# Performance work log

Hardware: AMD Instinct MI355X
Metric: run time of the kernel (lower is better)

Reference implementation:

```python
import jax, jax.numpy as jnp
import numpy as np

IN_DIMS = 32
HID = 64
N_HIDDEN = 5  # tcnn n_hidden_layers = hidden_layers + 1 = 5
OUT_DIMS = 3
BATCH = 2097152


def setup_inputs() -> dict:
    key = jax.random.key(0)
    ks = jax.random.split(key, N_HIDDEN + 2)
    x = jax.random.normal(ks[0], (BATCH, IN_DIMS), dtype=jnp.float32)
    # tcnn FullyFusedMLP has no biases; Kaiming-ish init scale
    W0 = jax.random.normal(ks[1], (IN_DIMS, HID), dtype=jnp.float32) * (1.0 / np.sqrt(IN_DIMS))
    Wh = jax.random.normal(ks[2], (N_HIDDEN - 1, HID, HID), dtype=jnp.float32) * (1.0 / np.sqrt(HID))
    Wo = jax.random.normal(ks[3], (HID, OUT_DIMS), dtype=jnp.float32) * (1.0 / np.sqrt(HID))
    return {"x": x, "W0": W0, "Wh": Wh, "Wo": Wo}


def reference(x, W0, Wh, Wo):
    # input layer -> ReLU
    h = jax.nn.relu(x @ W0)  # [B, 64]
    # 4 more hidden layers of 64->64 with ReLU (small fixed count, unrolled)
    for i in range(Wh.shape[0]):
        h = jax.nn.relu(h @ Wh[i])
    # linear output layer (output_activation = None)
    return h @ Wo  # [B, 3]
```

## Files before the change

kernel.cpp:

```cpp
#include <hip/hip_runtime.h>


typedef __attribute__((ext_vector_type(8))) short short8;
typedef __attribute__((ext_vector_type(4))) float f32x4;

#define BATCH   2097152
#define NBLOCKS 1024
#define WAVES   (NBLOCKS * 4)
#define ROWS_PW 32
#define ITERS   (BATCH / (WAVES * ROWS_PW))
static_assert(BATCH == (size_t)WAVES * ROWS_PW * ITERS, "");

__device__ __forceinline__ unsigned cvt_pk(float a, float b) {
    unsigned r;
    asm("v_cvt_pk_bf16_f32 %0, %1, %2" : "=v"(r) : "v"(a), "v"(b));
    return r;
}

__global__ __launch_bounds__(256, 2)
void mlp_fused(const float* __restrict__ x, const float* __restrict__ W0,
               const float* __restrict__ Wh, const float* __restrict__ Wo,
               float* __restrict__ out)
{
    const int tid  = threadIdx.x;
    const int w    = tid >> 6;
    const int lane = tid & 63;
    const int n = lane & 15;
    const int q = lane >> 4;

    int phi[4];
    #pragma unroll
    for (int t = 0; t < 4; ++t)
        phi[t] = 32 * (t >> 1) + 8 * (n >> 2) + 4 * (t & 1) + (n & 3);

    short8 wf0[4], wfh[4][4][2], wfo[2];
    #pragma unroll
    for (int t = 0; t < 4; ++t) {
        const float* p = W0 + (8 * q) * 64 + phi[t];
        union { unsigned u[4]; short8 s; } f;
        #pragma unroll
        for (int i = 0; i < 4; ++i)
            f.u[i] = cvt_pk(p[(2 * i) * 64], p[(2 * i + 1) * 64]);
        wf0[t] = f.s;
    }
    #pragma unroll
    for (int l = 0; l < 4; ++l)
        #pragma unroll
        for (int t = 0; t < 4; ++t)
            #pragma unroll
            for (int c = 0; c < 2; ++c) {
                const float* p = Wh + l * 4096 + (32 * c + 8 * q) * 64 + phi[t];
                union { unsigned u[4]; short8 s; } f;
                #pragma unroll
                for (int i = 0; i < 4; ++i)
                    f.u[i] = cvt_pk(p[(2 * i) * 64], p[(2 * i + 1) * 64]);
                wfh[l][t][c] = f.s;
            }
    #pragma unroll
    for (int c = 0; c < 2; ++c) {
        union { unsigned u[4]; short8 s; } f;
        #pragma unroll
        for (int i = 0; i < 4; ++i) {
            float a = (n < 3) ? Wo[(32 * c + 8 * q + 2 * i)     * 3 + n] : 0.f;
            float b = (n < 3) ? Wo[(32 * c + 8 * q + 2 * i + 1) * 3 + n] : 0.f;
            f.u[i] = cvt_pk(a, b);
        }
        wfo[c] = f.s;
    }

    const int gw = blockIdx.x * 4 + w;
    const f32x4 z = {0.f, 0.f, 0.f, 0.f};

    f32x4 rawA[2], rawB[2];
    auto issue_x = [&](int it) {
        const size_t r = ((size_t)it * WAVES + gw) * ROWS_PW;
        const f32x4* pA = (const f32x4*)(x + (r + n) * 32) + 2 * q;
        rawA[0] = pA[0]; rawA[1] = pA[1];
        const f32x4* pB = (const f32x4*)(x + (r + 16 + n) * 32) + 2 * q;
        rawB[0] = pB[0]; rawB[1] = pB[1];
    };
    auto convert_x = [&](const f32x4* raw) -> short8 {
        union { unsigned u[4]; short8 s; } f;
        f.u[0] = cvt_pk(raw[0][0], raw[0][1]);
        f.u[1] = cvt_pk(raw[0][2], raw[0][3]);
        f.u[2] = cvt_pk(raw[1][0], raw[1][1]);
        f.u[3] = cvt_pk(raw[1][2], raw[1][3]);
        return f.s;
    };
    auto packact = [&](const f32x4 (&acc)[4], short8& b0, short8& b1) {
        union { unsigned u[4]; short8 s; } A, B;
        A.u[0] = cvt_pk(fmaxf(acc[0][0], 0.f), fmaxf(acc[0][1], 0.f));
        A.u[1] = cvt_pk(fmaxf(acc[0][2], 0.f), fmaxf(acc[0][3], 0.f));
        A.u[2] = cvt_pk(fmaxf(acc[1][0], 0.f), fmaxf(acc[1][1], 0.f));
        A.u[3] = cvt_pk(fmaxf(acc[1][2], 0.f), fmaxf(acc[1][3], 0.f));
        B.u[0] = cvt_pk(fmaxf(acc[2][0], 0.f), fmaxf(acc[2][1], 0.f));
        B.u[1] = cvt_pk(fmaxf(acc[2][2], 0.f), fmaxf(acc[2][3], 0.f));
        B.u[2] = cvt_pk(fmaxf(acc[3][0], 0.f), fmaxf(acc[3][1], 0.f));
        B.u[3] = cvt_pk(fmaxf(acc[3][2], 0.f), fmaxf(acc[3][3], 0.f));
        b0 = A.s; b1 = B.s;
    };

    issue_x(0);

    #pragma unroll 1
    for (int it = 0; it < ITERS; ++it) {
        const short8 xfA = convert_x(rawA);
        const short8 xfB = convert_x(rawB);
        if (it + 1 < ITERS) issue_x(it + 1);

        const size_t row0 = ((size_t)it * WAVES + gw) * ROWS_PW;

        f32x4 accA[4], accB[4];
        #pragma unroll
        for (int t = 0; t < 4; ++t)
            accA[t] = __builtin_amdgcn_mfma_f32_16x16x32_bf16(wf0[t], xfA, z, 0, 0, 0);
        #pragma unroll
        for (int t = 0; t < 4; ++t)
            accB[t] = __builtin_amdgcn_mfma_f32_16x16x32_bf16(wf0[t], xfB, z, 0, 0, 0);

        #pragma unroll
        for (int s = 0; s < 4; ++s) {
            short8 a0, a1, c0, c1;
            packact(accA, a0, a1);
            packact(accB, c0, c1);
            #pragma unroll
            for (int t = 0; t < 4; ++t)
                accA[t] = __builtin_amdgcn_mfma_f32_16x16x32_bf16(
                              wfh[s][t][0], a0, z, 0, 0, 0);
            #pragma unroll
            for (int t = 0; t < 4; ++t)
                accA[t] = __builtin_amdgcn_mfma_f32_16x16x32_bf16(
                              wfh[s][t][1], a1, accA[t], 0, 0, 0);
            #pragma unroll
            for (int t = 0; t < 4; ++t)
                accB[t] = __builtin_amdgcn_mfma_f32_16x16x32_bf16(
                              wfh[s][t][0], c0, z, 0, 0, 0);
            #pragma unroll
            for (int t = 0; t < 4; ++t)
                accB[t] = __builtin_amdgcn_mfma_f32_16x16x32_bf16(
                              wfh[s][t][1], c1, accB[t], 0, 0, 0);
        }

        {
            short8 a0, a1, c0, c1;
            packact(accA, a0, a1);
            packact(accB, c0, c1);
            f32x4 oA = __builtin_amdgcn_mfma_f32_16x16x32_bf16(wfo[0], a0, z, 0, 0, 0);
            oA = __builtin_amdgcn_mfma_f32_16x16x32_bf16(wfo[1], a1, oA, 0, 0, 0);
            f32x4 oB = __builtin_amdgcn_mfma_f32_16x16x32_bf16(wfo[0], c0, z, 0, 0, 0);
            oB = __builtin_amdgcn_mfma_f32_16x16x32_bf16(wfo[1], c1, oB, 0, 0, 0);
            if (lane < 16) {
                float* pA = out + (row0 + lane) * 3;
                pA[0] = oA[0]; pA[1] = oA[1]; pA[2] = oA[2];
                float* pB = out + (row0 + 16 + lane) * 3;
                pB[0] = oB[0]; pB[1] = oB[1]; pB[2] = oB[2];
            }
        }
    }
}

extern "C" void kernel_launch(void* const* d_in, const int* in_sizes, int n_in,
                              void* d_out, int out_size, void* d_ws, size_t ws_size,
                              hipStream_t stream) {
    (void)in_sizes; (void)n_in; (void)d_ws; (void)ws_size; (void)out_size;
    const float* x  = (const float*)d_in[0];
    const float* W0 = (const float*)d_in[1];
    const float* Wh = (const float*)d_in[2];
    const float* Wo = (const float*)d_in[3];
    float* out = (float*)d_out;
    mlp_fused<<<NBLOCKS, 256, 0, stream>>>(x, W0, Wh, Wo, out);
}
```

Before: 383.2 us.

## Stage bf16 weight fragments in LDS and halve rows per wave for occupancy

Weight fragments are no longer held in registers for the whole kernel. They are converted once per block into a 38-entry LDS table, with the conversion work split across the four waves. Each iteration streams them back from LDS with double-buffered X/Y registers. Each wave now processes 16 rows per iteration instead of 32, and launch bounds rise to 4 blocks per CU to increase occupancy and latency hiding. The cost is LDS read traffic and a block barrier, plus less independent MFMA work per wave to cover dependency chains.

```diff
diff --git a/kernel.cpp b/kernel.cpp
--- a/kernel.cpp
+++ b/kernel.cpp
@@ -6,10 +6,9 @@
 
 #define BATCH   2097152
 #define NBLOCKS 1024
-#define WAVES   (NBLOCKS * 4)
-#define ROWS_PW 32
-#define ITERS   (BATCH / (WAVES * ROWS_PW))
-static_assert(BATCH == (size_t)WAVES * ROWS_PW * ITERS, "");
+#define NWAVES  (NBLOCKS * 4)
+#define ITERS   (BATCH / (NWAVES * 16))
+static_assert(BATCH == (size_t)NWAVES * 16 * ITERS, "");
 
 __device__ __forceinline__ unsigned cvt_pk(float a, float b) {
     unsigned r;
@@ -17,76 +16,77 @@
     return r;
 }
 
-__global__ __launch_bounds__(256, 2)
+__global__ __launch_bounds__(256, 4)
 void mlp_fused(const float* __restrict__ x, const float* __restrict__ W0,
                const float* __restrict__ Wh, const float* __restrict__ Wo,
                float* __restrict__ out)
 {
+    __shared__ short8 wlds[38][64];
+
     const int tid  = threadIdx.x;
     const int w    = tid >> 6;
     const int lane = tid & 63;
     const int n = lane & 15;
     const int q = lane >> 4;
 
+    const int gw = blockIdx.x * 4 + w;
+
+    f32x4 raw0, raw1;
+    {
+        const f32x4* p = (const f32x4*)(x + ((size_t)gw * 16 + n) * 32) + 2 * q;
+        raw0 = p[0]; raw1 = p[1];
+    }
+
     int phi[4];
     #pragma unroll
     for (int t = 0; t < 4; ++t)
         phi[t] = 32 * (t >> 1) + 8 * (n >> 2) + 4 * (t & 1) + (n & 3);
 
-    short8 wf0[4], wfh[4][4][2], wfo[2];
-    #pragma unroll
-    for (int t = 0; t < 4; ++t) {
-        const float* p = W0 + (8 * q) * 64 + phi[t];
+    auto build = [&](const float* p) -> short8 {
         union { unsigned u[4]; short8 s; } f;
         #pragma unroll
         for (int i = 0; i < 4; ++i)
             f.u[i] = cvt_pk(p[(2 * i) * 64], p[(2 * i + 1) * 64]);
-        wf0[t] = f.s;
-    }
-    #pragma unroll
-    for (int l = 0; l < 4; ++l)
+        return f.s;
+    };
+    if (w == 0) {
+        #pragma unroll
+        for (int t = 0; t < 4; ++t)
+            wlds[t][lane] = build(W0 + (8 * q) * 64 + phi[t]);
         #pragma unroll
         for (int t = 0; t < 4; ++t)
             #pragma unroll
-            for (int c = 0; c < 2; ++c) {
-                const float* p = Wh + l * 4096 + (32 * c + 8 * q) * 64 + phi[t];
-                union { unsigned u[4]; short8 s; } f;
-                #pragma unroll
-                for (int i = 0; i < 4; ++i)
-                    f.u[i] = cvt_pk(p[(2 * i) * 64], p[(2 * i + 1) * 64]);
-                wfh[l][t][c] = f.s;
+            for (int c = 0; c < 2; ++c)
+                wlds[28 + 2 * t + c][lane] =
+                    build(Wh + 3 * 4096 + (32 * c + 8 * q) * 64 + phi[t]);
+        #pragma unroll
+        for (int c = 0; c < 2; ++c) {
+            union { unsigned u[4]; short8 s; } f;
+            #pragma unroll
+            for (int i = 0; i < 4; ++i) {
+                float a = (n < 3) ? Wo[(32 * c + 8 * q + 2 * i)     * 3 + n] : 0.f;
+                float b = (n < 3) ? Wo[(32 * c + 8 * q + 2 * i + 1) * 3 + n] : 0.f;
+                f.u[i] = cvt_pk(a, b);
             }
+            wlds[36 + c][lane] = f.s;
+        }
+    } else {
+        const int l = w - 1;
+        #pragma unroll
+        for (int t = 0; t < 4; ++t)
+            #pragma unroll
+            for (int c = 0; c < 2; ++c)
+                wlds[4 + 8 * l + 2 * t + c][lane] =
+                    build(Wh + l * 4096 + (32 * c + 8 * q) * 64 + phi[t]);
+    }
+    __syncthreads();
+
+    const f32x4 z = {0.f, 0.f, 0.f, 0.f};
+    short8 X[8], Y[8];
+
     #pragma unroll
-    for (int c = 0; c < 2; ++c) {
-        union { unsigned u[4]; short8 s; } f;
-        #pragma unroll
-        for (int i = 0; i < 4; ++i) {
-            float a = (n < 3) ? Wo[(32 * c + 8 * q + 2 * i)     * 3 + n] : 0.f;
-            float b = (n < 3) ? Wo[(32 * c + 8 * q + 2 * i + 1) * 3 + n] : 0.f;
-            f.u[i] = cvt_pk(a, b);
-        }
-        wfo[c] = f.s;
-    }
+    for (int j = 0; j < 4; ++j) X[j] = wlds[j][lane];
 
-    const int gw = blockIdx.x * 4 + w;
-    const f32x4 z = {0.f, 0.f, 0.f, 0.f};
-
-    f32x4 rawA[2], rawB[2];
-    auto issue_x = [&](int it) {
-        const size_t r = ((size_t)it * WAVES + gw) * ROWS_PW;
-        const f32x4* pA = (const f32x4*)(x + (r + n) * 32) + 2 * q;
-        rawA[0] = pA[0]; rawA[1] = pA[1];
-        const f32x4* pB = (const f32x4*)(x + (r + 16 + n) * 32) + 2 * q;
-        rawB[0] = pB[0]; rawB[1] = pB[1];
-    };
-    auto convert_x = [&](const f32x4* raw) -> short8 {
-        union { unsigned u[4]; short8 s; } f;
-        f.u[0] = cvt_pk(raw[0][0], raw[0][1]);
-        f.u[1] = cvt_pk(raw[0][2], raw[0][3]);
-        f.u[2] = cvt_pk(raw[1][0], raw[1][1]);
-        f.u[3] = cvt_pk(raw[1][2], raw[1][3]);
-        return f.s;
-    };
     auto packact = [&](const f32x4 (&acc)[4], short8& b0, short8& b1) {
         union { unsigned u[4]; short8 s; } A, B;
         A.u[0] = cvt_pk(fmaxf(acc[0][0], 0.f), fmaxf(acc[0][1], 0.f));
@@ -100,61 +100,79 @@
         b0 = A.s; b1 = B.s;
     };
 
-    issue_x(0);
-
     #pragma unroll 1
     for (int it = 0; it < ITERS; ++it) {
-        const short8 xfA = convert_x(rawA);
-        const short8 xfB = convert_x(rawB);
-        if (it + 1 < ITERS) issue_x(it + 1);
+        short8 xf;
+        {
+            union { unsigned u[4]; short8 s; } f;
+            f.u[0] = cvt_pk(raw0[0], raw0[1]); f.u[1] = cvt_pk(raw0[2], raw0[3]);
+            f.u[2] = cvt_pk(raw1[0], raw1[1]); f.u[3] = cvt_pk(raw1[2], raw1[3]);
+            xf = f.s;
+        }
+        if (it + 1 < ITERS) {
+            const size_t r = ((size_t)(it + 1) * NWAVES + gw) * 16;
+            const f32x4* p = (const f32x4*)(x + (r + n) * 32) + 2 * q;
+            raw0 = p[0]; raw1 = p[1];
+        }
+        const size_t row0 = ((size_t)it * NWAVES + gw) * 16;
 
-        const size_t row0 = ((size_t)it * WAVES + gw) * ROWS_PW;
+        f32x4 acc[4];
+        short8 b0, b1;
 
-        f32x4 accA[4], accB[4];
+        #pragma unroll
+        for (int j = 0; j < 8; ++j) Y[j] = wlds[4 + j][lane];
         #pragma unroll
         for (int t = 0; t < 4; ++t)
-            accA[t] = __builtin_amdgcn_mfma_f32_16x16x32_bf16(wf0[t], xfA, z, 0, 0, 0);
+            acc[t] = __builtin_amdgcn_mfma_f32_16x16x32_bf16(X[t], xf, z, 0, 0, 0);
+
+        #pragma unroll
+        for (int j = 0; j < 8; ++j) X[j] = wlds[12 + j][lane];
+        packact(acc, b0, b1);
         #pragma unroll
         for (int t = 0; t < 4; ++t)
-            accB[t] = __builtin_amdgcn_mfma_f32_16x16x32_bf16(wf0[t], xfB, z, 0, 0, 0);
+            acc[t] = __builtin_amdgcn_mfma_f32_16x16x32_bf16(Y[2 * t], b0, z, 0, 0, 0);
+        #pragma unroll
+        for (int t = 0; t < 4; ++t)
+            acc[t] = __builtin_amdgcn_mfma_f32_16x16x32_bf16(Y[2 * t + 1], b1, acc[t], 0, 0, 0);
 
         #pragma unroll
-        for (int s = 0; s < 4; ++s) {
-            short8 a0, a1, c0, c1;
-            packact(accA, a0, a1);
-            packact(accB, c0, c1);
-            #pragma unroll
-            for (int t = 0; t < 4; ++t)
-                accA[t] = __builtin_amdgcn_mfma_f32_16x16x32_bf16(
-                              wfh[s][t][0], a0, z, 0, 0, 0);
-            #pragma unroll
-            for (int t = 0; t < 4; ++t)
-                accA[t] = __builtin_amdgcn_mfma_f32_16x16x32_bf16(
-                              wfh[s][t][1], a1, accA[t], 0, 0, 0);
-            #pragma unroll
-            for (int t = 0; t < 4; ++t)
-                accB[t] = __builtin_amdgcn_mfma_f32_16x16x32_bf16(
-                              wfh[s][t][0], c0, z, 0, 0, 0);
-            #pragma unroll
-            for (int t = 0; t < 4; ++t)
-                accB[t] = __builtin_amdgcn_mfma_f32_16x16x32_bf16(
-                              wfh[s][t][1], c1, accB[t], 0, 0, 0);
-        }
+        for (int j = 0; j < 8; ++j) Y[j] = wlds[20 + j][lane];
+        packact(acc, b0, b1);
+        #pragma unroll
+        for (int t = 0; t < 4; ++t)
+            acc[t] = __builtin_amdgcn_mfma_f32_16x16x32_bf16(X[2 * t], b0, z, 0, 0, 0);
+        #pragma unroll
+        for (int t = 0; t < 4; ++t)
+            acc[t] = __builtin_amdgcn_mfma_f32_16x16x32_bf16(X[2 * t + 1], b1, acc[t], 0, 0, 0);
 
-        {
-            short8 a0, a1, c0, c1;
-            packact(accA, a0, a1);
-            packact(accB, c0, c1);
-            f32x4 oA = __builtin_amdgcn_mfma_f32_16x16x32_bf16(wfo[0], a0, z, 0, 0, 0);
-            oA = __builtin_amdgcn_mfma_f32_16x16x32_bf16(wfo[1], a1, oA, 0, 0, 0);
-            f32x4 oB = __builtin_amdgcn_mfma_f32_16x16x32_bf16(wfo[0], c0, z, 0, 0, 0);
-            oB = __builtin_amdgcn_mfma_f32_16x16x32_bf16(wfo[1], c1, oB, 0, 0, 0);
-            if (lane < 16) {
-                float* pA = out + (row0 + lane) * 3;
-                pA[0] = oA[0]; pA[1] = oA[1]; pA[2] = oA[2];
-                float* pB = out + (row0 + 16 + lane) * 3;
-                pB[0] = oB[0]; pB[1] = oB[1]; pB[2] = oB[2];
-            }
+        #pragma unroll
+        for (int j = 0; j < 8; ++j) X[j] = wlds[28 + j][lane];
+        packact(acc, b0, b1);
+        #pragma unroll
+        for (int t = 0; t < 4; ++t)
+            acc[t] = __builtin_amdgcn_mfma_f32_16x16x32_bf16(Y[2 * t], b0, z, 0, 0, 0);
+        #pragma unroll
+        for (int t = 0; t < 4; ++t)
+            acc[t] = __builtin_amdgcn_mfma_f32_16x16x32_bf16(Y[2 * t + 1], b1, acc[t], 0, 0, 0);
+
+        Y[0] = wlds[36][lane];
+        Y[1] = wlds[37][lane];
+        packact(acc, b0, b1);
+        #pragma unroll
+        for (int t = 0; t < 4; ++t)
+            acc[t] = __builtin_amdgcn_mfma_f32_16x16x32_bf16(X[2 * t], b0, z, 0, 0, 0);
+        #pragma unroll
+        for (int t = 0; t < 4; ++t)
+            acc[t] = __builtin_amdgcn_mfma_f32_16x16x32_bf16(X[2 * t + 1], b1, acc[t], 0, 0, 0);
+
+        #pragma unroll
+        for (int j = 0; j < 4; ++j) X[j] = wlds[j][lane];
+        packact(acc, b0, b1);
+        f32x4 o = __builtin_amdgcn_mfma_f32_16x16x32_bf16(Y[0], b0, z, 0, 0, 0);
+        o = __builtin_amdgcn_mfma_f32_16x16x32_bf16(Y[1], b1, o, 0, 0, 0);
+        if (lane < 16) {
+            float* po = out + (row0 + lane) * 3;
+            po[0] = o[0]; po[1] = o[1]; po[2] = o[2];
         }
     }
 }
```

After: 377.4 us. Within noise of the previous version (-1.5%).
